# Kernel tuning notes

Measured on AMD Instinct MI355X. Metric: run time of the kernel, lower is better.

Reference implementation:

```python
import jax, jax.numpy as jnp
import numpy as np
from jax import lax

_GRAY = jnp.array([0.299, 0.587, 0.114], dtype=jnp.float32)  # cv2 RGB2GRAY weights


def _conv(x, w, b):
    # x: [B,C,H,W], w: [O,I,kh,kw], SAME padding (matches padding=k//2 for odd k)
    y = lax.conv_general_dilated(x, w, (1, 1), 'SAME',
                                 dimension_numbers=('NCHW', 'OIHW', 'NCHW'))
    return y + b[None, :, None, None]


def _maxpool2(x):
    return lax.reduce_window(x, -jnp.inf, lax.max, (1, 1, 2, 2), (1, 1, 2, 2), 'VALID')


def _resize_bilinear(img, out_h, out_w):
    # cv2.resize INTER_LINEAR semantics: half-pixel-centered bilinear sampling, edge clamped
    B, C, H, W = img.shape
    ys = jnp.clip((jnp.arange(out_h, dtype=jnp.float32) + 0.5) * (H / out_h) - 0.5, 0.0, H - 1)
    xs = jnp.clip((jnp.arange(out_w, dtype=jnp.float32) + 0.5) * (W / out_w) - 0.5, 0.0, W - 1)
    y0 = jnp.floor(ys).astype(jnp.int32)
    x0 = jnp.floor(xs).astype(jnp.int32)
    y1 = jnp.minimum(y0 + 1, H - 1)
    x1 = jnp.minimum(x0 + 1, W - 1)
    wy = (ys - y0.astype(jnp.float32))[None, None, :, None]
    wx = (xs - x0.astype(jnp.float32))[None, None, None, :]
    r0 = img[:, :, y0, :]
    r1 = img[:, :, y1, :]
    rows = r0 * (1.0 - wy) + r1 * wy          # [B,C,out_h,W]
    c0 = rows[:, :, :, x0]
    c1 = rows[:, :, :, x1]
    return c0 * (1.0 - wx) + c1 * wx          # [B,C,out_h,out_w]


def _forward(input, w1, b1, w2, b2, w3, b3, w4, b4, w5, b5):
    x = jax.nn.relu(_conv(input, w1, b1))
    x = _maxpool2(x)
    x = jax.nn.relu(_conv(x, w2, b2))
    x = _maxpool2(x)
    x = jax.nn.relu(_conv(x, w3, b3))
    x = jax.nn.relu(_conv(x, w4, b4))
    x = _conv(x, w5, b5)                       # [B,1,H/4,W/4]
    out_h, out_w = x.shape[2], x.shape[3]
    # rgb2gray path is detached in the original (detach().cpu()): stop_gradient
    gray = jnp.einsum('bchw,c->bhw', lax.stop_gradient(input), _GRAY)[:, None]  # [B,1,H,W]
    gray = _resize_bilinear(gray, out_h, out_w)
    return jax.nn.relu(x + jax.nn.relu(gray))


def setup_inputs() -> dict:
    key = jax.random.key(0)
    ks = jax.random.split(key, 12)
    B, H, W = 8, 768, 1024
    def w(k, shape, fan_in):
        return (jax.random.normal(k, shape, dtype=jnp.float32) / np.sqrt(fan_in)).astype(jnp.float32)
    return {
        'input': jax.random.normal(ks[0], (B, 3, H, W), dtype=jnp.float32),
        'w1': w(ks[1], (20, 3, 7, 7), 3 * 49),  'b1': jnp.zeros((20,), jnp.float32),
        'w2': w(ks[2], (40, 20, 5, 5), 20 * 25), 'b2': jnp.zeros((40,), jnp.float32),
        'w3': w(ks[3], (20, 40, 5, 5), 40 * 25), 'b3': jnp.zeros((20,), jnp.float32),
        'w4': w(ks[4], (10, 20, 5, 5), 20 * 25), 'b4': jnp.zeros((10,), jnp.float32),
        'w5': w(ks[5], (1, 10, 1, 1), 10),       'b5': jnp.zeros((1,), jnp.float32),
    }


def reference(input, w1, b1, w2, b2, w3, b3, w4, b4, w5, b5):
    return _forward(input, w1, b1, w2, b2, w3, b3, w4, b4, w5, b5)
```

## Files before the change

kernel.cpp:

```cpp
#include <hip/hip_runtime.h>


typedef _Float16 half_t;
typedef _Float16 half8 __attribute__((ext_vector_type(8)));
typedef float floatx4 __attribute__((ext_vector_type(4)));

#define IN_H 768
#define IN_W 1024
#define P1H 384
#define P1W 512
#define P2H 192
#define P2W 256

#define OFF_P2 0ULL
#define OFF_P1 44040192ULL
#define OFF_X3 44040192ULL
#define OFF_W2 119537664ULL
#define OFF_W3 119691264ULL
#define OFF_W4 119896064ULL
#define OFF_W1 119947264ULL

union PK4 { half_t h[4]; uint2 u; };
union U8 { half8 v; uint2 u[2]; };

__global__ __launch_bounds__(256) void pack_weights(
    const float* __restrict__ w2, const float* __restrict__ w3,
    const float* __restrict__ w4, const float* __restrict__ w1,
    half_t* __restrict__ wp2, half_t* __restrict__ wp3, half_t* __restrict__ wp4,
    half_t* __restrict__ wp1)
{
  int t = blockIdx.x * 256 + threadIdx.x;
  if (t < 38400) {
    int tap = t / 1536, r = t % 1536, oc = r >> 5, c = r & 31;
    float v = (oc < 40 && c < 20) ? w2[(oc * 20 + c) * 25 + tap] : 0.f;
    wp2[t] = (half_t)v;
  } else if (t < 89600) {
    int u = t - 38400;
    int tap = u / 2048, r = u % 2048, oc = r >> 6, c = r & 63;
    float v = (oc < 20 && c < 40) ? w3[(oc * 40 + c) * 25 + tap] : 0.f;
    wp3[u] = (half_t)v;
  } else if (t < 102400) {
    int u = t - 89600;
    int tap = u / 512, r = u % 512, oc = r >> 5, c = r & 31;
    float v = (oc < 10 && c < 20) ? w4[(oc * 20 + c) * 25 + tap] : 0.f;
    wp4[u] = (half_t)v;
  } else if (t < 109568) {
    int u = t - 102400;
    int ky = u / 1024, r = u % 1024, oc = r >> 5, k = r & 31;
    int kx = k >> 2, c = k & 3;
    float v = (oc < 20 && c < 3 && kx < 7) ? w1[((oc * 3 + c) * 7 + ky) * 7 + kx] : 0.f;
    wp1[u] = (half_t)v;
  }
}

__global__ __launch_bounds__(256) void conv1_mfma(
    const float* __restrict__ in, const half_t* __restrict__ wp,
    const float* __restrict__ bias, half_t* __restrict__ P1)
{
  __shared__ __align__(16) half_t ltile[38 * 40 * 4];
  const int b = blockIdx.z, ty0 = blockIdx.y * 32, tx0 = blockIdx.x * 32;
  const int tid = threadIdx.x;
  const int HW1 = IN_H * IN_W;

  const float* p0 = in + (size_t)b * 3 * HW1;
  const bool interior = (blockIdx.x >= 1) && (blockIdx.x <= 30) &&
                        (blockIdx.y >= 1) && (blockIdx.y <= 22);
  if (interior) {
    for (int i = tid; i < 380; i += 256) {
      int r = i / 10, c4 = i - r * 10;
      const float* pr = p0 + (size_t)(ty0 - 3 + r) * IN_W + (tx0 - 4 + 4 * c4);
      float4 v0 = *(const float4*)(pr);
      float4 v1 = *(const float4*)(pr + HW1);
      float4 v2 = *(const float4*)(pr + 2 * HW1);
      PK4 a0, a1, a2, a3;
      a0.h[0] = (half_t)v0.x; a0.h[1] = (half_t)v1.x; a0.h[2] = (half_t)v2.x; a0.h[3] = (half_t)0.f;
      a1.h[0] = (half_t)v0.y; a1.h[1] = (half_t)v1.y; a1.h[2] = (half_t)v2.y; a1.h[3] = (half_t)0.f;
      a2.h[0] = (half_t)v0.z; a2.h[1] = (half_t)v1.z; a2.h[2] = (half_t)v2.z; a2.h[3] = (half_t)0.f;
      a3.h[0] = (half_t)v0.w; a3.h[1] = (half_t)v1.w; a3.h[2] = (half_t)v2.w; a3.h[3] = (half_t)0.f;
      uint4* dst = (uint4*)(ltile + (r * 40 + 4 * c4) * 4);
      dst[0] = make_uint4(a0.u.x, a0.u.y, a1.u.x, a1.u.y);
      dst[1] = make_uint4(a2.u.x, a2.u.y, a3.u.x, a3.u.y);
    }
  } else {
    for (int i = tid; i < 1520; i += 256) {
      int r = i / 40, c = i - r * 40;
      int gy = ty0 - 3 + r, gx = tx0 - 4 + c;
      float v0 = 0.f, v1 = 0.f, v2 = 0.f;
      if (gy >= 0 && gy < IN_H && (unsigned)gx < (unsigned)IN_W) {
        size_t o = (size_t)gy * IN_W + gx;
        v0 = p0[o];
        v1 = p0[o + HW1];
        v2 = p0[o + 2 * HW1];
      }
      PK4 pk;
      pk.h[0] = (half_t)v0; pk.h[1] = (half_t)v1;
      pk.h[2] = (half_t)v2; pk.h[3] = (half_t)0.f;
      *(uint2*)(ltile + (r * 40 + c) * 4) = pk.u;
    }
  }
  __syncthreads();

  const int wv = tid >> 6, ln = tid & 63, q = ln >> 4, nl = ln & 15;
  const int cbase = (2 * nl + 2 * q + 1) * 4;
  const half_t* wA = wp + nl * 32 + q * 8;

  floatx4 bv[2];
  #pragma unroll
  for (int mt = 0; mt < 2; ++mt)
    #pragma unroll
    for (int r = 0; r < 4; ++r) {
      int oc = mt * 16 + q * 4 + r;
      bv[mt][r] = (oc < 20) ? bias[oc] : 0.f;
    }
  const int pc = (tx0 >> 1) + nl;

  #pragma unroll
  for (int p = 0; p < 2; ++p) {
    const int rbase = p * 16 + 4 * wv;
    U8 frag[4][2];
    #pragma unroll
    for (int d = 0; d < 4; ++d) {
      const half_t* rp = ltile + (rbase + d) * 160 + cbase;
      #pragma unroll
      for (int phx = 0; phx < 2; ++phx) {
        frag[d][phx].u[0] = *(const uint2*)(rp + phx * 4);
        frag[d][phx].u[1] = *(const uint2*)(rp + phx * 4 + 4);
      }
    }
    half8 Abuf[2][2];
    Abuf[0][0] = *(const half8*)(wA);
    Abuf[0][1] = *(const half8*)(wA + 512);
    floatx4 acc[2][8];
    #pragma unroll
    for (int mt = 0; mt < 2; ++mt)
      #pragma unroll
      for (int j = 0; j < 8; ++j) acc[mt][j] = (floatx4){0.f, 0.f, 0.f, 0.f};

    #pragma unroll
    for (int ky = 0; ky < 7; ++ky) {
      if (ky < 6) {
        Abuf[(ky + 1) & 1][0] = *(const half8*)(wA + (ky + 1) * 1024);
        Abuf[(ky + 1) & 1][1] = *(const half8*)(wA + (ky + 1) * 1024 + 512);
      }
      #pragma unroll
      for (int j = 0; j < 8; ++j) {
        const int g = j >> 2, ph = j & 3, phy = ph >> 1, phx = ph & 1;
        half8 B = frag[(2 * g + phy + ky) & 3][phx].v;
        acc[0][j] = __builtin_amdgcn_mfma_f32_16x16x32_f16(Abuf[ky & 1][0], B, acc[0][j], 0, 0, 0);
        acc[1][j] = __builtin_amdgcn_mfma_f32_16x16x32_f16(Abuf[ky & 1][1], B, acc[1][j], 0, 0, 0);
      }
      if (ky < 6) {
        const half_t* rp = ltile + (rbase + ky + 4) * 160 + cbase;
        #pragma unroll
        for (int phx = 0; phx < 2; ++phx) {
          frag[ky & 3][phx].u[0] = *(const uint2*)(rp + phx * 4);
          frag[ky & 3][phx].u[1] = *(const uint2*)(rp + phx * 4 + 4);
        }
      }
    }

    const int pr0 = (ty0 >> 1) + 8 * p + 2 * wv;
    #pragma unroll
    for (int g = 0; g < 2; ++g) {
      size_t pxbase = (((size_t)b * P1H + pr0 + g) * P1W + pc) * 24;
      PK4 pk0;
      #pragma unroll
      for (int r = 0; r < 4; ++r) {
        float x = fmaxf(fmaxf(acc[0][g * 4 + 0][r], acc[0][g * 4 + 1][r]),
                        fmaxf(acc[0][g * 4 + 2][r], acc[0][g * 4 + 3][r]));
        pk0.h[r] = (half_t)fmaxf(x + bv[0][r], 0.f);
      }
      *(uint2*)(P1 + pxbase + q * 4) = pk0.u;
      if (q < 2) {
        PK4 pk1;
        #pragma unroll
        for (int r = 0; r < 4; ++r) {
          float x = fmaxf(fmaxf(acc[1][g * 4 + 0][r], acc[1][g * 4 + 1][r]),
                          fmaxf(acc[1][g * 4 + 2][r], acc[1][g * 4 + 3][r]));
          pk1.h[r] = (half_t)fmaxf(x + bv[1][r], 0.f);
        }
        *(uint2*)(P1 + pxbase + 16 + q * 4) = pk1.u;
      }
    }
  }
}

__global__ __launch_bounds__(256, 2) void conv2_mfma(
    const half_t* __restrict__ P1, const half_t* __restrict__ wp,
    const float* __restrict__ bias, half_t* __restrict__ P2)
{
  __shared__ __align__(16) half_t lin[20 * 36 * 24 + 16];
  const int b = blockIdx.z, ty0 = blockIdx.y * 16, tx0 = blockIdx.x * 32;
  const int tid = threadIdx.x;
  if (tid < 16) lin[20 * 36 * 24 + tid] = (half_t)0.f;
  for (int i = tid; i < 2160; i += 256) {
    int px = i / 3, part = i - px * 3;
    int row = px / 36, col = px - row * 36;
    int gy = ty0 - 2 + row, gx = tx0 - 2 + col;
    uint4 v = make_uint4(0, 0, 0, 0);
    if (gy >= 0 && gy < P1H && (unsigned)gx < (unsigned)P1W)
      v = *(const uint4*)(P1 + (((size_t)b * P1H + gy) * P1W + gx) * 24 + part * 8);
    *(uint4*)(lin + px * 24 + part * 8) = v;
  }
  __syncthreads();

  const int wv = tid >> 6, ln = tid & 63, q = ln >> 4, nl = ln & 15;
  const int cbase = 2 * nl * 24 + q * 8;
  half8 frag[4][6];
  #pragma unroll
  for (int d = 0; d < 4; ++d) {
    const half_t* rp = lin + (4 * wv + d) * 864 + cbase;
    #pragma unroll
    for (int c = 0; c < 6; ++c) frag[d][c] = *(const half8*)(rp + c * 24);
  }
  const half_t* wA = wp + nl * 32 + q * 8;
  half8 Abuf[2][3];
  #pragma unroll
  for (int mt = 0; mt < 3; ++mt) Abuf[0][mt] = *(const half8*)(wA + mt * 512);
  floatx4 acc[3][8];
  #pragma unroll
  for (int mt = 0; mt < 3; ++mt)
    #pragma unroll
    for (int j = 0; j < 8; ++j) acc[mt][j] = (floatx4){0.f, 0.f, 0.f, 0.f};

  #pragma unroll
  for (int ky = 0; ky < 5; ++ky) {
    #pragma unroll
    for (int kx = 0; kx < 5; ++kx) {
      const int tap = ky * 5 + kx;
      if (tap < 24) {
        #pragma unroll
        for (int mt = 0; mt < 3; ++mt)
          Abuf[(tap + 1) & 1][mt] = *(const half8*)(wA + (tap + 1) * 1536 + mt * 512);
      }
      #pragma unroll
      for (int j = 0; j < 8; ++j) {
        const int g = j >> 2, ph = j & 3, phy = ph >> 1, phx = ph & 1;
        half8 B = frag[(2 * g + phy + ky) & 3][kx + phx];
        acc[0][j] = __builtin_amdgcn_mfma_f32_16x16x32_f16(Abuf[tap & 1][0], B, acc[0][j], 0, 0, 0);
        acc[1][j] = __builtin_amdgcn_mfma_f32_16x16x32_f16(Abuf[tap & 1][1], B, acc[1][j], 0, 0, 0);
        acc[2][j] = __builtin_amdgcn_mfma_f32_16x16x32_f16(Abuf[tap & 1][2], B, acc[2][j], 0, 0, 0);
      }
    }
    if (ky < 4) {
      const half_t* rp = lin + (4 * wv + ky + 4) * 864 + cbase;
      #pragma unroll
      for (int c = 0; c < 6; ++c) frag[ky & 3][c] = *(const half8*)(rp + c * 24);
    }
  }

  floatx4 bv[3];
  #pragma unroll
  for (int mt = 0; mt < 3; ++mt)
    #pragma unroll
    for (int r = 0; r < 4; ++r) {
      int oc = mt * 16 + q * 4 + r;
      bv[mt][r] = (oc < 40) ? bias[oc] : 0.f;
    }
  const int pr0 = (ty0 >> 1) + 2 * wv;
  const int pc = (tx0 >> 1) + nl;
  #pragma unroll
  for (int g = 0; g < 2; ++g) {
    size_t pxbase = (((size_t)b * P2H + pr0 + g) * P2W + pc) * 56;
    #pragma unroll
    for (int mt = 0; mt < 3; ++mt) {
      PK4 pk;
      #pragma unroll
      for (int r = 0; r < 4; ++r) {
        float x = fmaxf(fmaxf(acc[mt][g * 4 + 0][r], acc[mt][g * 4 + 1][r]),
                        fmaxf(acc[mt][g * 4 + 2][r], acc[mt][g * 4 + 3][r]));
        pk.h[r] = (half_t)fmaxf(x + bv[mt][r], 0.f);
      }
      *(uint2*)(P2 + pxbase + mt * 16 + q * 4) = pk.u;
    }
    if (q == 0)
      *(uint4*)(P2 + pxbase + 48) = make_uint4(0, 0, 0, 0);
  }
}

__global__ __launch_bounds__(256, 2) void conv3_mfma(
    const half_t* __restrict__ P2, const half_t* __restrict__ wp,
    const float* __restrict__ bias, half_t* __restrict__ X3)
{
  __shared__ __align__(16) half_t lin[12 * 36 * 56 + 16];
  const int b = blockIdx.z, ty0 = blockIdx.y * 8, tx0 = blockIdx.x * 32;
  const int tid = threadIdx.x;
  if (tid < 16) lin[12 * 36 * 56 + tid] = (half_t)0.f;
  for (int i = tid; i < 3024; i += 256) {
    int px = i / 7, part = i - px * 7;
    int row = px / 36, col = px - row * 36;
    int gy = ty0 - 2 + row, gx = tx0 - 2 + col;
    uint4 v = make_uint4(0, 0, 0, 0);
    if (gy >= 0 && gy < P2H && (unsigned)gx < (unsigned)P2W)
      v = *(const uint4*)(P2 + (((size_t)b * P2H + gy) * P2W + gx) * 56 + part * 8);
    *(uint4*)(lin + px * 56 + part * 8) = v;
  }
  __syncthreads();

  const int wv = tid >> 6, ln = tid & 63, q = ln >> 4, nl = ln & 15;
  const int cbase = 2 * nl * 56 + q * 8;
  half8 frag[2][6][2];
  #pragma unroll
  for (int c = 0; c < 6; ++c)
    #pragma unroll
    for (int cb = 0; cb < 2; ++cb) {
      frag[0][c][cb] = *(const half8*)(lin + (2 * wv + 0) * 2016 + cbase + c * 56 + cb * 32);
      frag[1][c][cb] = *(const half8*)(lin + (2 * wv + 1) * 2016 + cbase + c * 56 + cb * 32);
    }
  const half_t* wA = wp + nl * 64 + q * 8;
  half8 Abuf[2][2][2];
  #pragma unroll
  for (int mt = 0; mt < 2; ++mt)
    #pragma unroll
    for (int cb = 0; cb < 2; ++cb)
      Abuf[0][mt][cb] = *(const half8*)(wA + mt * 1024 + cb * 32);
  floatx4 acc[2][4];
  #pragma unroll
  for (int mt = 0; mt < 2; ++mt)
    #pragma unroll
    for (int j = 0; j < 4; ++j) acc[mt][j] = (floatx4){0.f, 0.f, 0.f, 0.f};

  #pragma unroll
  for (int ky = 0; ky < 5; ++ky) {
    #pragma unroll
    for (int kx = 0; kx < 5; ++kx) {
      const int tap = ky * 5 + kx;
      if (tap < 24) {
        #pragma unroll
        for (int mt = 0; mt < 2; ++mt)
          #pragma unroll
          for (int cb = 0; cb < 2; ++cb)
            Abuf[(tap + 1) & 1][mt][cb] =
                *(const half8*)(wA + (tap + 1) * 2048 + mt * 1024 + cb * 32);
      }
      #pragma unroll
      for (int cb = 0; cb < 2; ++cb)
        #pragma unroll
        for (int j = 0; j < 4; ++j) {
          const int phy = j >> 1, phx = j & 1;
          half8 B = frag[(ky + phy) & 1][kx + phx][cb];
          acc[0][j] = __builtin_amdgcn_mfma_f32_16x16x32_f16(Abuf[tap & 1][0][cb], B, acc[0][j], 0, 0, 0);
          acc[1][j] = __builtin_amdgcn_mfma_f32_16x16x32_f16(Abuf[tap & 1][1][cb], B, acc[1][j], 0, 0, 0);
        }
    }
    if (ky < 4) {
      const half_t* rp = lin + (2 * wv + ky + 2) * 2016 + cbase;
      #pragma unroll
      for (int c = 0; c < 6; ++c)
        #pragma unroll
        for (int cb = 0; cb < 2; ++cb)
          frag[ky & 1][c][cb] = *(const half8*)(rp + c * 56 + cb * 32);
    }
  }

  floatx4 bv[2];
  #pragma unroll
  for (int mt = 0; mt < 2; ++mt)
    #pragma unroll
    for (int r = 0; r < 4; ++r) {
      int oc = mt * 16 + q * 4 + r;
      bv[mt][r] = (oc < 20) ? bias[oc] : 0.f;
    }
  #pragma unroll
  for (int j = 0; j < 4; ++j) {
    const int phy = j >> 1, phx = j & 1;
    int y = ty0 + 2 * wv + phy, x = tx0 + 2 * nl + phx;
    size_t pxbase = (((size_t)b * P2H + y) * P2W + x) * 24;
    #pragma unroll
    for (int mt = 0; mt < 2; ++mt) {
      if (mt == 1 && q >= 2) continue;
      floatx4 v = acc[mt][j];
      PK4 pk;
      #pragma unroll
      for (int r = 0; r < 4; ++r) pk.h[r] = (half_t)fmaxf(v[r] + bv[mt][r], 0.f);
      *(uint2*)(X3 + pxbase + mt * 16 + q * 4) = pk.u;
    }
  }
}

__global__ __launch_bounds__(256, 2) void conv4_mfma(
    const half_t* __restrict__ X3, const half_t* __restrict__ wp,
    const float* __restrict__ bias, const float* __restrict__ w5,
    const float* __restrict__ b5, const float* __restrict__ in,
    float* __restrict__ out)
{
  __shared__ __align__(16) half_t lin[20 * 36 * 24 + 16];
  const int b = blockIdx.z, ty0 = blockIdx.y * 16, tx0 = blockIdx.x * 32;
  const int tid = threadIdx.x;
  if (tid < 16) lin[20 * 36 * 24 + tid] = (half_t)0.f;
  for (int i = tid; i < 2160; i += 256) {
    int px = i / 3, part = i - px * 3;
    int row = px / 36, col = px - row * 36;
    int gy = ty0 - 2 + row, gx = tx0 - 2 + col;
    uint4 v = make_uint4(0, 0, 0, 0);
    if (gy >= 0 && gy < P2H && (unsigned)gx < (unsigned)P2W)
      v = *(const uint4*)(X3 + (((size_t)b * P2H + gy) * P2W + gx) * 24 + part * 8);
    *(uint4*)(lin + px * 24 + part * 8) = v;
  }
  __syncthreads();

  const int wv = tid >> 6, ln = tid & 63, q = ln >> 4, nl = ln & 15;
  const int cbase = 2 * nl * 24 + q * 8;
  half8 frag[4][6];
  #pragma unroll
  for (int d = 0; d < 4; ++d) {
    const half_t* rp = lin + (4 * wv + d) * 864 + cbase;
    #pragma unroll
    for (int c = 0; c < 6; ++c) frag[d][c] = *(const half8*)(rp + c * 24);
  }
  const half_t* wA = wp + nl * 32 + q * 8;
  half8 Abuf[2];
  Abuf[0] = *(const half8*)(wA);
  floatx4 acc[8];
  #pragma unroll
  for (int j = 0; j < 8; ++j) acc[j] = (floatx4){0.f, 0.f, 0.f, 0.f};

  #pragma unroll
  for (int ky = 0; ky < 5; ++ky) {
    #pragma unroll
    for (int kx = 0; kx < 5; ++kx) {
      const int tap = ky * 5 + kx;
      if (tap < 24) Abuf[(tap + 1) & 1] = *(const half8*)(wA + (tap + 1) * 512);
      #pragma unroll
      for (int j = 0; j < 8; ++j) {
        const int g = j >> 2, ph = j & 3, phy = ph >> 1, phx = ph & 1;
        half8 B = frag[(2 * g + phy + ky) & 3][kx + phx];
        acc[j] = __builtin_amdgcn_mfma_f32_16x16x32_f16(Abuf[tap & 1], B, acc[j], 0, 0, 0);
      }
    }
    if (ky < 4) {
      const half_t* rp = lin + (4 * wv + ky + 4) * 864 + cbase;
      #pragma unroll
      for (int c = 0; c < 6; ++c) frag[ky & 3][c] = *(const half8*)(rp + c * 24);
    }
  }

  float bv[4], w5v[4];
  #pragma unroll
  for (int r = 0; r < 4; ++r) {
    int oc = q * 4 + r;
    bv[r]  = (oc < 10) ? bias[oc] : 0.f;
    w5v[r] = (oc < 10) ? w5[oc] : 0.f;
  }
  const float b5v = b5[0];
  const float* inb = in + (size_t)b * 3 * (IN_H * IN_W);

  #pragma unroll
  for (int g = 0; g < 2; ++g)
    #pragma unroll
    for (int phy = 0; phy < 2; ++phy) {
      const int y = ty0 + 4 * wv + 2 * g + phy;
      const int x0 = tx0 + 2 * nl;
      float s0 = 0.f, s1 = 0.f;
      #pragma unroll
      for (int r = 0; r < 4; ++r) {
        s0 += w5v[r] * fmaxf(acc[g * 4 + 2 * phy + 0][r] + bv[r], 0.f);
        s1 += w5v[r] * fmaxf(acc[g * 4 + 2 * phy + 1][r] + bv[r], 0.f);
      }
      s0 += __shfl_xor(s0, 16); s0 += __shfl_xor(s0, 32);
      s1 += __shfl_xor(s1, 16); s1 += __shfl_xor(s1, 32);
      if (q == 0) {
        const size_t cb = (size_t)(4 * y + 1) * IN_W + 4 * x0;
        float g0 = 0.f, g1 = 0.f;
        #pragma unroll
        for (int ch = 0; ch < 3; ++ch) {
          const float coef = (ch == 0) ? 0.299f : ((ch == 1) ? 0.587f : 0.114f);
          const float* qp = inb + (size_t)ch * (IN_H * IN_W);
          float4 a0 = *(const float4*)(qp + cb);
          float4 a1 = *(const float4*)(qp + cb + 4);
          float4 d0 = *(const float4*)(qp + cb + IN_W);
          float4 d1 = *(const float4*)(qp + cb + IN_W + 4);
          g0 += coef * (a0.y + a0.z + d0.y + d0.z);
          g1 += coef * (a1.y + a1.z + d1.y + d1.z);
        }
        float o0 = fmaxf(s0 + b5v + fmaxf(g0 * 0.25f, 0.f), 0.f);
        float o1 = fmaxf(s1 + b5v + fmaxf(g1 * 0.25f, 0.f), 0.f);
        *(float2*)(out + ((size_t)b * P2H + y) * P2W + x0) = make_float2(o0, o1);
      }
    }
}

extern "C" void kernel_launch(void* const* d_in, const int* in_sizes, int n_in,
                              void* d_out, int out_size, void* d_ws, size_t ws_size,
                              hipStream_t stream) {
  const float* input = (const float*)d_in[0];
  const float* w1 = (const float*)d_in[1];  const float* b1 = (const float*)d_in[2];
  const float* w2 = (const float*)d_in[3];  const float* b2 = (const float*)d_in[4];
  const float* w3 = (const float*)d_in[5];  const float* b3 = (const float*)d_in[6];
  const float* w4 = (const float*)d_in[7];  const float* b4 = (const float*)d_in[8];
  const float* w5 = (const float*)d_in[9];  const float* b5 = (const float*)d_in[10];
  float* out = (float*)d_out;
  char* ws = (char*)d_ws;

  half_t* P2h = (half_t*)(ws + OFF_P2);
  half_t* P1h = (half_t*)(ws + OFF_P1);
  half_t* X3h = (half_t*)(ws + OFF_X3);
  half_t* wp2 = (half_t*)(ws + OFF_W2);
  half_t* wp3 = (half_t*)(ws + OFF_W3);
  half_t* wp4 = (half_t*)(ws + OFF_W4);
  half_t* wp1 = (half_t*)(ws + OFF_W1);

  pack_weights<<<432, 256, 0, stream>>>(w2, w3, w4, w1, wp2, wp3, wp4, wp1);
  conv1_mfma<<<dim3(32, 24, 8), 256, 0, stream>>>(input, wp1, b1, P1h);
  conv2_mfma<<<dim3(16, 24, 8), 256, 0, stream>>>(P1h, wp2, b2, P2h);
  conv3_mfma<<<dim3(8, 24, 8), 256, 0, stream>>>(P2h, wp3, b3, X3h);
  conv4_mfma<<<dim3(8, 12, 8), 256, 0, stream>>>(X3h, wp4, b4, w5, b5, input, out);
}
```

Measured before the change: 379.3 us.

## Load conv2/conv4 input fragments directly from global memory instead of LDS

```diff
diff --git a/kernel.cpp b/kernel.cpp
--- a/kernel.cpp
+++ b/kernel.cpp
@@ -22,6 +22,13 @@
 
 union PK4 { half_t h[4]; uint2 u; };
 union U8 { half8 v; uint2 u[2]; };
+
+__device__ __forceinline__ half8 h8zero() {
+  half8 z;
+  #pragma unroll
+  for (int i = 0; i < 8; ++i) z[i] = (half_t)0.f;
+  return z;
+}
 
 __global__ __launch_bounds__(256) void pack_weights(
     const float* __restrict__ w2, const float* __restrict__ w3,
@@ -189,30 +196,37 @@
     const half_t* __restrict__ P1, const half_t* __restrict__ wp,
     const float* __restrict__ bias, half_t* __restrict__ P2)
 {
-  __shared__ __align__(16) half_t lin[20 * 36 * 24 + 16];
   const int b = blockIdx.z, ty0 = blockIdx.y * 16, tx0 = blockIdx.x * 32;
   const int tid = threadIdx.x;
-  if (tid < 16) lin[20 * 36 * 24 + tid] = (half_t)0.f;
-  for (int i = tid; i < 2160; i += 256) {
-    int px = i / 3, part = i - px * 3;
-    int row = px / 36, col = px - row * 36;
-    int gy = ty0 - 2 + row, gx = tx0 - 2 + col;
-    uint4 v = make_uint4(0, 0, 0, 0);
-    if (gy >= 0 && gy < P1H && (unsigned)gx < (unsigned)P1W)
-      v = *(const uint4*)(P1 + (((size_t)b * P1H + gy) * P1W + gx) * 24 + part * 8);
-    *(uint4*)(lin + px * 24 + part * 8) = v;
-  }
-  __syncthreads();
-
   const int wv = tid >> 6, ln = tid & 63, q = ln >> 4, nl = ln & 15;
-  const int cbase = 2 * nl * 24 + q * 8;
+
+  const bool interior = (blockIdx.x >= 1) && (blockIdx.x <= 14) &&
+                        (blockIdx.y >= 1) && (blockIdx.y <= 22);
+  const int RS = P1W * 24;
+  const half_t* gb = P1 + (((size_t)b * P1H + (ty0 - 2)) * P1W + (tx0 - 2 + 2 * nl)) * 24 + q * 8;
+
   half8 frag[4][6];
-  #pragma unroll
-  for (int d = 0; d < 4; ++d) {
-    const half_t* rp = lin + (4 * wv + d) * 864 + cbase;
-    #pragma unroll
-    for (int c = 0; c < 6; ++c) frag[d][c] = *(const half8*)(rp + c * 24);
-  }
+  if (interior) {
+    #pragma unroll
+    for (int d = 0; d < 4; ++d) {
+      const half_t* rp = gb + (4 * wv + d) * RS;
+      #pragma unroll
+      for (int c = 0; c < 6; ++c) frag[d][c] = *(const half8*)(rp + c * 24);
+    }
+  } else {
+    #pragma unroll
+    for (int d = 0; d < 4; ++d) {
+      const int gy = ty0 - 2 + 4 * wv + d;
+      #pragma unroll
+      for (int c = 0; c < 6; ++c) {
+        const int gx = tx0 - 2 + 2 * nl + c;
+        frag[d][c] = ((unsigned)gy < (unsigned)P1H && (unsigned)gx < (unsigned)P1W)
+            ? *(const half8*)(P1 + (((size_t)b * P1H + gy) * P1W + gx) * 24 + q * 8)
+            : h8zero();
+      }
+    }
+  }
+
   const half_t* wA = wp + nl * 32 + q * 8;
   half8 Abuf[2][3];
   #pragma unroll
@@ -243,9 +257,21 @@
       }
     }
     if (ky < 4) {
-      const half_t* rp = lin + (4 * wv + ky + 4) * 864 + cbase;
-      #pragma unroll
-      for (int c = 0; c < 6; ++c) frag[ky & 3][c] = *(const half8*)(rp + c * 24);
+      const int rr = 4 * wv + ky + 4;
+      if (interior) {
+        const half_t* rp = gb + rr * RS;
+        #pragma unroll
+        for (int c = 0; c < 6; ++c) frag[ky & 3][c] = *(const half8*)(rp + c * 24);
+      } else {
+        const int gy = ty0 - 2 + rr;
+        #pragma unroll
+        for (int c = 0; c < 6; ++c) {
+          const int gx = tx0 - 2 + 2 * nl + c;
+          frag[ky & 3][c] = ((unsigned)gy < (unsigned)P1H && (unsigned)gx < (unsigned)P1W)
+              ? *(const half8*)(P1 + (((size_t)b * P1H + gy) * P1W + gx) * 24 + q * 8)
+              : h8zero();
+        }
+      }
     }
   }
 
@@ -384,30 +410,37 @@
     const float* __restrict__ b5, const float* __restrict__ in,
     float* __restrict__ out)
 {
-  __shared__ __align__(16) half_t lin[20 * 36 * 24 + 16];
   const int b = blockIdx.z, ty0 = blockIdx.y * 16, tx0 = blockIdx.x * 32;
   const int tid = threadIdx.x;
-  if (tid < 16) lin[20 * 36 * 24 + tid] = (half_t)0.f;
-  for (int i = tid; i < 2160; i += 256) {
-    int px = i / 3, part = i - px * 3;
-    int row = px / 36, col = px - row * 36;
-    int gy = ty0 - 2 + row, gx = tx0 - 2 + col;
-    uint4 v = make_uint4(0, 0, 0, 0);
-    if (gy >= 0 && gy < P2H && (unsigned)gx < (unsigned)P2W)
-      v = *(const uint4*)(X3 + (((size_t)b * P2H + gy) * P2W + gx) * 24 + part * 8);
-    *(uint4*)(lin + px * 24 + part * 8) = v;
-  }
-  __syncthreads();
-
   const int wv = tid >> 6, ln = tid & 63, q = ln >> 4, nl = ln & 15;
-  const int cbase = 2 * nl * 24 + q * 8;
+
+  const bool interior = (blockIdx.x >= 1) && (blockIdx.x <= 6) &&
+                        (blockIdx.y >= 1) && (blockIdx.y <= 10);
+  const int RS = P2W * 24;
+  const half_t* gb = X3 + (((size_t)b * P2H + (ty0 - 2)) * P2W + (tx0 - 2 + 2 * nl)) * 24 + q * 8;
+
   half8 frag[4][6];
-  #pragma unroll
-  for (int d = 0; d < 4; ++d) {
-    const half_t* rp = lin + (4 * wv + d) * 864 + cbase;
-    #pragma unroll
-    for (int c = 0; c < 6; ++c) frag[d][c] = *(const half8*)(rp + c * 24);
-  }
+  if (interior) {
+    #pragma unroll
+    for (int d = 0; d < 4; ++d) {
+      const half_t* rp = gb + (4 * wv + d) * RS;
+      #pragma unroll
+      for (int c = 0; c < 6; ++c) frag[d][c] = *(const half8*)(rp + c * 24);
+    }
+  } else {
+    #pragma unroll
+    for (int d = 0; d < 4; ++d) {
+      const int gy = ty0 - 2 + 4 * wv + d;
+      #pragma unroll
+      for (int c = 0; c < 6; ++c) {
+        const int gx = tx0 - 2 + 2 * nl + c;
+        frag[d][c] = ((unsigned)gy < (unsigned)P2H && (unsigned)gx < (unsigned)P2W)
+            ? *(const half8*)(X3 + (((size_t)b * P2H + gy) * P2W + gx) * 24 + q * 8)
+            : h8zero();
+      }
+    }
+  }
+
   const half_t* wA = wp + nl * 32 + q * 8;
   half8 Abuf[2];
   Abuf[0] = *(const half8*)(wA);
@@ -429,9 +462,21 @@
       }
     }
     if (ky < 4) {
-      const half_t* rp = lin + (4 * wv + ky + 4) * 864 + cbase;
-      #pragma unroll
-      for (int c = 0; c < 6; ++c) frag[ky & 3][c] = *(const half8*)(rp + c * 24);
+      const int rr = 4 * wv + ky + 4;
+      if (interior) {
+        const half_t* rp = gb + rr * RS;
+        #pragma unroll
+        for (int c = 0; c < 6; ++c) frag[ky & 3][c] = *(const half8*)(rp + c * 24);
+      } else {
+        const int gy = ty0 - 2 + rr;
+        #pragma unroll
+        for (int c = 0; c < 6; ++c) {
+          const int gx = tx0 - 2 + 2 * nl + c;
+          frag[ky & 3][c] = ((unsigned)gy < (unsigned)P2H && (unsigned)gx < (unsigned)P2W)
+              ? *(const half8*)(X3 + (((size_t)b * P2H + gy) * P2W + gx) * 24 + q * 8)
+              : h8zero();
+        }
+      }
     }
   }
 
```

Result: slower. 405.1 us (+6.8%).

## Fold horizontal taps into the K dimension for conv2 and conv4 MFMA

Applied to the files above, without the earlier changes.

```diff
diff --git a/kernel.cpp b/kernel.cpp
--- a/kernel.cpp
+++ b/kernel.cpp
@@ -16,9 +16,9 @@
 #define OFF_P1 44040192ULL
 #define OFF_X3 44040192ULL
 #define OFF_W2 119537664ULL
-#define OFF_W3 119691264ULL
-#define OFF_W4 119896064ULL
-#define OFF_W1 119947264ULL
+#define OFF_W3 119599104ULL
+#define OFF_W4 119803904ULL
+#define OFF_W1 119824384ULL
 
 union PK4 { half_t h[4]; uint2 u; };
 union U8 { half8 v; uint2 u[2]; };
@@ -30,22 +30,26 @@
     half_t* __restrict__ wp1)
 {
   int t = blockIdx.x * 256 + threadIdx.x;
-  if (t < 38400) {
-    int tap = t / 1536, r = t % 1536, oc = r >> 5, c = r & 31;
-    float v = (oc < 40 && c < 20) ? w2[(oc * 20 + c) * 25 + tap] : 0.f;
+  if (t < 30720) {
+    int ky = t / 6144, r = t % 6144;
+    int kk = r / 1536, r2 = r % 1536, oc = r2 >> 5, k = r2 & 31;
+    int o = kk * 32 + k, p = o / 24, c = o % 24;
+    float v = (oc < 40 && c < 20 && p < 5) ? w2[(oc * 20 + c) * 25 + ky * 5 + p] : 0.f;
     wp2[t] = (half_t)v;
-  } else if (t < 89600) {
-    int u = t - 38400;
+  } else if (t < 81920) {
+    int u = t - 30720;
     int tap = u / 2048, r = u % 2048, oc = r >> 6, c = r & 63;
     float v = (oc < 20 && c < 40) ? w3[(oc * 40 + c) * 25 + tap] : 0.f;
     wp3[u] = (half_t)v;
-  } else if (t < 102400) {
-    int u = t - 89600;
-    int tap = u / 512, r = u % 512, oc = r >> 5, c = r & 31;
-    float v = (oc < 10 && c < 20) ? w4[(oc * 20 + c) * 25 + tap] : 0.f;
+  } else if (t < 92160) {
+    int u = t - 81920;
+    int ky = u / 2048, r = u % 2048;
+    int kk = r / 512, r2 = r % 512, oc = r2 >> 5, k = r2 & 31;
+    int o = kk * 32 + k, p = o / 24, c = o % 24;
+    float v = (oc < 10 && c < 20 && p < 5) ? w4[(oc * 20 + c) * 25 + ky * 5 + p] : 0.f;
     wp4[u] = (half_t)v;
-  } else if (t < 109568) {
-    int u = t - 102400;
+  } else if (t < 99328) {
+    int u = t - 92160;
     int ky = u / 1024, r = u % 1024, oc = r >> 5, k = r & 31;
     int kx = k >> 2, c = k & 3;
     float v = (oc < 20 && c < 3 && kx < 7) ? w1[((oc * 3 + c) * 7 + ky) * 7 + kx] : 0.f;
@@ -205,18 +209,9 @@
   __syncthreads();
 
   const int wv = tid >> 6, ln = tid & 63, q = ln >> 4, nl = ln & 15;
-  const int cbase = 2 * nl * 24 + q * 8;
-  half8 frag[4][6];
-  #pragma unroll
-  for (int d = 0; d < 4; ++d) {
-    const half_t* rp = lin + (4 * wv + d) * 864 + cbase;
-    #pragma unroll
-    for (int c = 0; c < 6; ++c) frag[d][c] = *(const half8*)(rp + c * 24);
-  }
+  const half_t* cb0 = lin + 2 * nl * 24 + q * 8;
   const half_t* wA = wp + nl * 32 + q * 8;
-  half8 Abuf[2][3];
-  #pragma unroll
-  for (int mt = 0; mt < 3; ++mt) Abuf[0][mt] = *(const half8*)(wA + mt * 512);
+
   floatx4 acc[3][8];
   #pragma unroll
   for (int mt = 0; mt < 3; ++mt)
@@ -226,26 +221,19 @@
   #pragma unroll
   for (int ky = 0; ky < 5; ++ky) {
     #pragma unroll
-    for (int kx = 0; kx < 5; ++kx) {
-      const int tap = ky * 5 + kx;
-      if (tap < 24) {
-        #pragma unroll
-        for (int mt = 0; mt < 3; ++mt)
-          Abuf[(tap + 1) & 1][mt] = *(const half8*)(wA + (tap + 1) * 1536 + mt * 512);
-      }
+    for (int kk = 0; kk < 4; ++kk) {
+      const half_t* wt = wA + (ky * 4 + kk) * 1536;
+      half8 A0 = *(const half8*)(wt);
+      half8 A1 = *(const half8*)(wt + 512);
+      half8 A2 = *(const half8*)(wt + 1024);
       #pragma unroll
       for (int j = 0; j < 8; ++j) {
-        const int g = j >> 2, ph = j & 3, phy = ph >> 1, phx = ph & 1;
-        half8 B = frag[(2 * g + phy + ky) & 3][kx + phx];
-        acc[0][j] = __builtin_amdgcn_mfma_f32_16x16x32_f16(Abuf[tap & 1][0], B, acc[0][j], 0, 0, 0);
-        acc[1][j] = __builtin_amdgcn_mfma_f32_16x16x32_f16(Abuf[tap & 1][1], B, acc[1][j], 0, 0, 0);
-        acc[2][j] = __builtin_amdgcn_mfma_f32_16x16x32_f16(Abuf[tap & 1][2], B, acc[2][j], 0, 0, 0);
-      }
-    }
-    if (ky < 4) {
-      const half_t* rp = lin + (4 * wv + ky + 4) * 864 + cbase;
-      #pragma unroll
-      for (int c = 0; c < 6; ++c) frag[ky & 3][c] = *(const half8*)(rp + c * 24);
+        const int g = j >> 2, phy = (j >> 1) & 1, phx = j & 1;
+        half8 B = *(const half8*)(cb0 + (4 * wv + 2 * g + phy + ky) * 864 + phx * 24 + kk * 32);
+        acc[0][j] = __builtin_amdgcn_mfma_f32_16x16x32_f16(A0, B, acc[0][j], 0, 0, 0);
+        acc[1][j] = __builtin_amdgcn_mfma_f32_16x16x32_f16(A1, B, acc[1][j], 0, 0, 0);
+        acc[2][j] = __builtin_amdgcn_mfma_f32_16x16x32_f16(A2, B, acc[2][j], 0, 0, 0);
+      }
     }
   }
 
@@ -400,17 +388,9 @@
   __syncthreads();
 
   const int wv = tid >> 6, ln = tid & 63, q = ln >> 4, nl = ln & 15;
-  const int cbase = 2 * nl * 24 + q * 8;
-  half8 frag[4][6];
-  #pragma unroll
-  for (int d = 0; d < 4; ++d) {
-    const half_t* rp = lin + (4 * wv + d) * 864 + cbase;
-    #pragma unroll
-    for (int c = 0; c < 6; ++c) frag[d][c] = *(const half8*)(rp + c * 24);
-  }
+  const half_t* cb0 = lin + 2 * nl * 24 + q * 8;
   const half_t* wA = wp + nl * 32 + q * 8;
-  half8 Abuf[2];
-  Abuf[0] = *(const half8*)(wA);
+
   floatx4 acc[8];
   #pragma unroll
   for (int j = 0; j < 8; ++j) acc[j] = (floatx4){0.f, 0.f, 0.f, 0.f};
@@ -418,20 +398,14 @@
   #pragma unroll
   for (int ky = 0; ky < 5; ++ky) {
     #pragma unroll
-    for (int kx = 0; kx < 5; ++kx) {
-      const int tap = ky * 5 + kx;
-      if (tap < 24) Abuf[(tap + 1) & 1] = *(const half8*)(wA + (tap + 1) * 512);
+    for (int kk = 0; kk < 4; ++kk) {
+      half8 A = *(const half8*)(wA + (ky * 4 + kk) * 512);
       #pragma unroll
       for (int j = 0; j < 8; ++j) {
-        const int g = j >> 2, ph = j & 3, phy = ph >> 1, phx = ph & 1;
-        half8 B = frag[(2 * g + phy + ky) & 3][kx + phx];
-        acc[j] = __builtin_amdgcn_mfma_f32_16x16x32_f16(Abuf[tap & 1], B, acc[j], 0, 0, 0);
-      }
-    }
-    if (ky < 4) {
-      const half_t* rp = lin + (4 * wv + ky + 4) * 864 + cbase;
-      #pragma unroll
-      for (int c = 0; c < 6; ++c) frag[ky & 3][c] = *(const half8*)(rp + c * 24);
+        const int g = j >> 2, phy = (j >> 1) & 1, phx = j & 1;
+        half8 B = *(const half8*)(cb0 + (4 * wv + 2 * g + phy + ky) * 864 + phx * 24 + kk * 32);
+        acc[j] = __builtin_amdgcn_mfma_f32_16x16x32_f16(A, B, acc[j], 0, 0, 0);
+      }
     }
   }
 
@@ -500,7 +474,7 @@
   half_t* wp4 = (half_t*)(ws + OFF_W4);
   half_t* wp1 = (half_t*)(ws + OFF_W1);
 
-  pack_weights<<<432, 256, 0, stream>>>(w2, w3, w4, w1, wp2, wp3, wp4, wp1);
+  pack_weights<<<388, 256, 0, stream>>>(w2, w3, w4, w1, wp2, wp3, wp4, wp1);
   conv1_mfma<<<dim3(32, 24, 8), 256, 0, stream>>>(input, wp1, b1, P1h);
   conv2_mfma<<<dim3(16, 24, 8), 256, 0, stream>>>(P1h, wp2, b2, P2h);
   conv3_mfma<<<dim3(8, 24, 8), 256, 0, stream>>>(P2h, wp3, b3, X3h);
```

Measured after the change: 365.2 us. 1.04x faster.
